# Kernel optimization log

Measured on AMD Instinct MI355X. Metric: run time of the kernel, lower is better.

Reference implementation:

```python
import jax, jax.numpy as jnp
import numpy as np

B, N = 4, 500
C_DIM = 256            # content_dim == feat_channels
G = 4                  # n_groups
P_IN, P_OUT = 32, 128
EFF = C_DIM // G       # 64 = eff_in_dim = eff_out_dim
TOTAL = EFF * EFF + P_IN * P_OUT   # 8192 params per group per query
STRIDES = (8, 16, 32, 64)
LVL_SHAPES = ((100, 160), (50, 80), (25, 40), (13, 20))
TAU = 2.0
LVL_MAP = 3.0          # log2(STRIDES[0]): z -> fpn level index
EPS = 1e-5


def setup_inputs() -> dict:
    key = jax.random.key(0)
    ks = jax.random.split(key, 16)
    feats = [jax.random.normal(ks[i], (B, C_DIM, h, w), jnp.float32)
             for i, (h, w) in enumerate(LVL_SHAPES)]
    query_feat = jax.random.normal(ks[4], (B, N, C_DIM), jnp.float32)
    xy = jax.random.uniform(ks[5], (B, N, 2), jnp.float32, 50.0, 1000.0)
    z = jax.random.uniform(ks[6], (B, N, 1), jnp.float32, 3.0, 6.0)
    r = jax.random.uniform(ks[7], (B, N, 1), jnp.float32, -1.0, 1.0)
    query_xyzr = jnp.concatenate([xy, z, r], -1)
    w_off = jax.random.normal(ks[8], (C_DIM, P_IN * G * 3), jnp.float32) * 0.01
    b_off = jax.random.normal(ks[9], (P_IN * G * 3,), jnp.float32) * 0.1
    w_pg = jax.random.normal(ks[10], (C_DIM, G * TOTAL), jnp.float32) * 0.02
    b_pg = jax.random.normal(ks[11], (G * TOTAL,), jnp.float32) * 0.02
    w_out = jax.random.normal(ks[12], (G * P_OUT * EFF, C_DIM), jnp.float32) * 0.005
    b_out = jnp.zeros((C_DIM,), jnp.float32)
    ln_g = jnp.ones((C_DIM,), jnp.float32)
    ln_b = jnp.zeros((C_DIM,), jnp.float32)
    return dict(feat0=feats[0], feat1=feats[1], feat2=feats[2], feat3=feats[3],
                query_feat=query_feat, query_xyzr=query_xyzr,
                w_off=w_off, b_off=b_off, w_pg=w_pg, b_pg=b_pg,
                w_out=w_out, b_out=b_out, ln_g=ln_g, ln_b=ln_b)


def _ln2d(x):
    # F.layer_norm over last TWO dims, no affine
    mu = x.mean((-2, -1), keepdims=True)
    var = jnp.mean((x - mu) ** 2, (-2, -1), keepdims=True)
    return (x - mu) * jax.lax.rsqrt(var + EPS)


def _bilinear(feat, px, py):
    # torch grid_sample(bilinear, zeros padding, align_corners=False)
    # feat: [BG, H, W, Cg]; px, py: [BG, Q] pixel coords
    BGn, H, W, Cg = feat.shape
    fflat = feat.reshape(BGn, H * W, Cg)
    bidx = jnp.arange(BGn)[:, None]
    x0 = jnp.floor(px)
    y0 = jnp.floor(py)
    wx, wy = px - x0, py - y0
    x0i, y0i = x0.astype(jnp.int32), y0.astype(jnp.int32)

    def corner(xi, yi, w):
        valid = (xi >= 0) & (xi < W) & (yi >= 0) & (yi < H)
        idx = jnp.clip(yi, 0, H - 1) * W + jnp.clip(xi, 0, W - 1)
        return fflat[bidx, idx] * (w * valid)[..., None]

    return (corner(x0i, y0i, (1 - wx) * (1 - wy)) + corner(x0i + 1, y0i, wx * (1 - wy))
            + corner(x0i, y0i + 1, (1 - wx) * wy) + corner(x0i + 1, y0i + 1, wx * wy))


def _forward(feat0, feat1, feat2, feat3, query_feat, query_xyzr,
             w_off, b_off, w_pg, b_pg, w_out, b_out, ln_g, ln_b):
    feats = (feat0, feat1, feat2, feat3)
    # --- make_sample_points ---
    off = (query_feat @ w_off + b_off).reshape(B, N, G * P_IN, 3)
    cc = query_xyzr[..., :2]
    z = query_xyzr[..., 2:3]
    r = query_xyzr[..., 3:4]
    roi_wh = (2.0 ** z) * jnp.concatenate([2.0 ** (-0.5 * r), 2.0 ** (0.5 * r)], -1)  # [B,N,2]
    sample_xy = cc[:, :, None, :] + off[..., :2] * roi_wh[:, :, None, :]   # [B,N,G*P,2]
    sample_lvl = z[:, :, None, 0:1] + off[..., 2:3]                        # [B,N,G*P,1]

    # --- sampling_3d: softmax level weights ---
    lvl = sample_lvl[..., 0] - LVL_MAP                                     # [B,N,G*P]
    grid = jnp.arange(len(STRIDES), dtype=lvl.dtype)
    lw = jax.nn.softmax(-((lvl[..., None] - grid) ** 2) / TAU, axis=-1)    # [B,N,G*P,L]

    # regroup to per-group layout [B*G, N*P, ...]
    sx = sample_xy.reshape(B, N, G, P_IN, 2).transpose(0, 2, 1, 3, 4).reshape(B * G, N * P_IN, 2)
    lw_g = lw.reshape(B, N, G, P_IN, -1).transpose(0, 2, 1, 3, 4).reshape(B * G, N * P_IN, -1)

    sampled = jnp.zeros((B * G, N * P_IN, EFF), jnp.float32)
    for li, (feat, stride) in enumerate(zip(feats, STRIDES)):
        H, W = feat.shape[2], feat.shape[3]
        fg = feat.reshape(B * G, EFF, H, W).transpose(0, 2, 3, 1)  # [BG,H,W,EFF]
        nx = sx[..., 0] / (W * stride) * 2.0 - 1.0
        ny = sx[..., 1] / (H * stride) * 2.0 - 1.0
        px = (nx + 1.0) * 0.5 * W - 0.5
        py = (ny + 1.0) * 0.5 * H - 0.5
        sampled = sampled + _bilinear(fg, px, py) * lw_g[..., li][..., None]
    # [B,N,G,P,EFF]
    x = sampled.reshape(B, G, N, P_IN, EFF).transpose(0, 2, 1, 3, 4)

    # --- AdaptiveMixing ---
    params = (query_feat @ w_pg + b_pg).reshape(B * N, G, TOTAL)
    M = params[..., :EFF * EFF].reshape(B * N, G, EFF, EFF)
    S = params[..., EFF * EFF:].reshape(B * N, G, P_OUT, P_IN)
    out = x.reshape(B * N, G, P_IN, EFF)
    out = jax.nn.relu(_ln2d(jnp.einsum('bgpc,bgcd->bgpd', out, M)))  # channel mix
    out = jax.nn.relu(_ln2d(jnp.einsum('bgop,bgpd->bgod', S, out)))  # spatial mix
    out = out.reshape(B, N, G * P_OUT * EFF) @ w_out + b_out
    q = query_feat + out

    # --- final LayerNorm(content_dim) with affine ---
    mu = q.mean(-1, keepdims=True)
    var = jnp.mean((q - mu) ** 2, -1, keepdims=True)
    return (q - mu) * jax.lax.rsqrt(var + EPS) * ln_g + ln_b


def reference(feat0, feat1, feat2, feat3, query_feat, query_xyzr,
              w_off, b_off, w_pg, b_pg, w_out, b_out, ln_g, ln_b):
    return _forward(feat0, feat1, feat2, feat3, query_feat, query_xyzr,
                    w_off, b_off, w_pg, b_pg, w_out, b_out, ln_g, ln_b)
```

## Files before the change

### kernel.cpp

```cpp
#include <hip/hip_runtime.h>
#include <hip/hip_bf16.h>
#include <cstdint>
#include <cstddef>

#define DI __device__ __forceinline__

#define NN 500
#define NQ 2000
#define GTOT 32768
#define LN_EPS 1e-5f

typedef __attribute__((ext_vector_type(8))) short short8v;
typedef __attribute__((ext_vector_type(4))) float f32x4;
typedef const __attribute__((address_space(1))) void* gp1_t;
typedef __attribute__((address_space(3))) void* lp3_t;

DI unsigned short f2bf(float f){
  unsigned u = __float_as_uint(f);
  return (unsigned short)((u + 0x7fffu + ((u>>16)&1u)) >> 16);
}
DI float bf2f(unsigned short s){ return __uint_as_float(((unsigned)s)<<16); }

DI ushort4 cvt4(float4 a){
  ushort4 r; r.x=f2bf(a.x); r.y=f2bf(a.y); r.z=f2bf(a.z); r.w=f2bf(a.w); return r;
}

DI void bred256(float& s, float& s2, float* red, int tid){
  #pragma unroll
  for(int off=32; off; off>>=1){
    s  += __shfl_xor(s,  off, 64);
    s2 += __shfl_xor(s2, off, 64);
  }
  int w = tid>>6;
  if((tid&63)==0){ red[w*2]=s; red[w*2+1]=s2; }
  __syncthreads();
  s  = red[0]+red[2]+red[4]+red[6];
  s2 = red[1]+red[3]+red[5]+red[7];
  __syncthreads();
}

__global__ __launch_bounds__(384) void k_off(const float* __restrict__ qf,
    const float* __restrict__ xyzr, const float* __restrict__ w_off,
    const float* __restrict__ b_off, float2* __restrict__ xyb, float4* __restrict__ lwb){
  __shared__ float qs[8][256];
  __shared__ float os[8][384];
  int q0 = blockIdx.x*8, tid = threadIdx.x;
  for(int idx=tid; idx<2048; idx+=384){
    int qq = idx>>8, k = idx&255;
    qs[qq][k] = qf[(size_t)(q0+qq)*256 + k];
  }
  __syncthreads();
  {
    int j = tid;
    float acc[8];
    #pragma unroll
    for(int i=0;i<8;i++) acc[i]=0.f;
    for(int k=0;k<256;k++){
      float w = w_off[(size_t)k*384 + j];
      #pragma unroll
      for(int qq=0;qq<8;qq++) acc[qq] += qs[qq][k]*w;
    }
    float bb = b_off[j];
    #pragma unroll
    for(int qq=0;qq<8;qq++) os[qq][j] = acc[qq] + bb;
  }
  __syncthreads();
  for(int idx=tid; idx<1024; idx+=384){
    int qq = idx>>7, gp = idx&127;
    int q = q0+qq;
    float4 xr = *(const float4*)&xyzr[(size_t)q*4];
    float rw = exp2f(xr.z - 0.5f*xr.w);
    float rh = exp2f(xr.z + 0.5f*xr.w);
    float sx = xr.x + os[qq][gp*3+0]*rw;
    float sy = xr.y + os[qq][gp*3+1]*rh;
    float lvl = xr.z + os[qq][gp*3+2] - 3.0f;
    float d0=lvl, d1=lvl-1.f, d2=lvl-2.f, d3=lvl-3.f;
    float e0=-0.5f*d0*d0, e1=-0.5f*d1*d1, e2=-0.5f*d2*d2, e3=-0.5f*d3*d3;
    float m = fmaxf(fmaxf(e0,e1),fmaxf(e2,e3));
    float x0=expf(e0-m), x1=expf(e1-m), x2=expf(e2-m), x3=expf(e3-m);
    float inv = 1.f/(x0+x1+x2+x3);
    xyb[(size_t)q*128+gp] = make_float2(sx,sy);
    lwb[(size_t)q*128+gp] = make_float4(x0*inv, x1*inv, x2*inv, x3*inv);
  }
}

__global__ __launch_bounds__(256) void k_cvtqf(const float* __restrict__ qf,
    unsigned short* __restrict__ qfb){
  int idx = blockIdx.x*256 + threadIdx.x;
  size_t base = (size_t)idx*8;
  int row = idx >> 5;
  ushort4 lo, hi;
  if(row < NQ){
    float4 a = *(const float4*)(qf + base);
    float4 b = *(const float4*)(qf + base + 4);
    lo = cvt4(a); hi = cvt4(b);
  } else {
    lo.x=lo.y=lo.z=lo.w=0; hi.x=hi.y=hi.z=hi.w=0;
  }
  *(ushort4*)(qfb + base) = lo;
  *(ushort4*)(qfb + base + 4) = hi;
}

__global__ __launch_bounds__(256) void k_trcvt(const float* __restrict__ src,
    unsigned short* __restrict__ dst, int R, int C){
  int ctiles = C >> 6;
  int rt = blockIdx.x / ctiles, ct = blockIdx.x % ctiles;
  int r0 = rt<<6, c0 = ct<<6;
  int t = threadIdx.x;
  int tr = t >> 4, tc = t & 15;
  int r = r0 + tr*4, c = c0 + tc*4;
  float4 v0 = *(const float4*)(src + (size_t)(r+0)*C + c);
  float4 v1 = *(const float4*)(src + (size_t)(r+1)*C + c);
  float4 v2 = *(const float4*)(src + (size_t)(r+2)*C + c);
  float4 v3 = *(const float4*)(src + (size_t)(r+3)*C + c);
  ushort4 o0 = make_ushort4(f2bf(v0.x), f2bf(v1.x), f2bf(v2.x), f2bf(v3.x));
  ushort4 o1 = make_ushort4(f2bf(v0.y), f2bf(v1.y), f2bf(v2.y), f2bf(v3.y));
  ushort4 o2 = make_ushort4(f2bf(v0.z), f2bf(v1.z), f2bf(v2.z), f2bf(v3.z));
  ushort4 o3 = make_ushort4(f2bf(v0.w), f2bf(v1.w), f2bf(v2.w), f2bf(v3.w));
  *(ushort4*)(dst + (size_t)(c+0)*R + r) = o0;
  *(ushort4*)(dst + (size_t)(c+1)*R + r) = o1;
  *(ushort4*)(dst + (size_t)(c+2)*R + r) = o2;
  *(ushort4*)(dst + (size_t)(c+3)*R + r) = o3;
}

__global__ __launch_bounds__(256) void k_featT(const float* __restrict__ src,
    unsigned short* __restrict__ dst, int HW, int nb){
  int bg = blockIdx.x / nb, hb = blockIdx.x % nb;
  int b = bg >> 2, g = bg & 3;
  const float* s = src + ((size_t)(b*256 + g*64))*HW;
  unsigned short* d = dst + (size_t)bg*HW*64;
  int t = threadIdx.x;
  int tc = t >> 4, th = t & 15;
  int c = tc*4, hw = hb*64 + th*4;
  if(hw >= HW) return;
  float4 v0 = *(const float4*)(s + (size_t)(c+0)*HW + hw);
  float4 v1 = *(const float4*)(s + (size_t)(c+1)*HW + hw);
  float4 v2 = *(const float4*)(s + (size_t)(c+2)*HW + hw);
  float4 v3 = *(const float4*)(s + (size_t)(c+3)*HW + hw);
  ushort4 o0 = make_ushort4(f2bf(v0.x), f2bf(v1.x), f2bf(v2.x), f2bf(v3.x));
  ushort4 o1 = make_ushort4(f2bf(v0.y), f2bf(v1.y), f2bf(v2.y), f2bf(v3.y));
  ushort4 o2 = make_ushort4(f2bf(v0.z), f2bf(v1.z), f2bf(v2.z), f2bf(v3.z));
  ushort4 o3 = make_ushort4(f2bf(v0.w), f2bf(v1.w), f2bf(v2.w), f2bf(v3.w));
  *(ushort4*)(d + (size_t)(hw+0)*64 + c) = o0;
  *(ushort4*)(d + (size_t)(hw+1)*64 + c) = o1;
  *(ushort4*)(d + (size_t)(hw+2)*64 + c) = o2;
  *(ushort4*)(d + (size_t)(hw+3)*64 + c) = o3;
}

DI f32x4 mfma16(short8v a, short8v b, f32x4 c){
  return __builtin_amdgcn_mfma_f32_16x16x32_bf16(a, b, c, 0, 0, 0);
}

DI int swz32(int c, int r){ return c ^ (r&3) ^ ((r>>2)&3); }

DI void stageG32(const unsigned short* __restrict__ g, size_t row0, size_t ldk,
                 size_t k0, unsigned short* lds, int tid){
  int wv = tid>>6;
  #pragma unroll
  for(int i=0;i<2;i++){
    int e = i*256 + tid;
    int r = e>>2, c = e&3;
    int cs = swz32(c, r);
    const unsigned short* gp = g + (row0 + (size_t)r)*ldk + k0 + (size_t)cs*8;
    unsigned short* lp = lds + (size_t)(i*256 + wv*64)*8;
    __builtin_amdgcn_global_load_lds((gp1_t)(const void*)gp, (lp3_t)(void*)lp, 16, 0, 0);
  }
}

DI short8v frag32(const unsigned short* lds, int row, int q4){
  return *(const short8v*)(lds + (size_t)row*32 + (size_t)swz32(q4, row)*8);
}

DI void mma32(const unsigned short* lsA, const unsigned short* lsB,
              int wm, int wn, int lane, f32x4 acc[4][4]){
  int r15 = lane&15, q4 = lane>>4;
  short8v a[4], b[4];
  #pragma unroll
  for(int i=0;i<4;i++){
    a[i] = frag32(lsA, wm*64 + i*16 + r15, q4);
    b[i] = frag32(lsB, wn*64 + i*16 + r15, q4);
  }
  #pragma unroll
  for(int mi=0;mi<4;mi++)
    #pragma unroll
    for(int ni=0;ni<4;ni++)
      acc[mi][ni] = mfma16(a[mi], b[ni], acc[mi][ni]);
}

DI int xcd_remap(int bid, int nwg){
  return ((bid & 7) * (nwg >> 3)) + (bid >> 3);
}

__global__ __launch_bounds__(256, 4) void k_pgemm_mfma(const unsigned short* __restrict__ qfb,
    const unsigned short* __restrict__ wpgT, const float* __restrict__ b_pg,
    unsigned short* __restrict__ par, int qbase, int qlim, int mtiles){
  __shared__ unsigned short pool[16384];
  int bid = xcd_remap(blockIdx.x, gridDim.x);
  int mt = bid % mtiles, nt = bid / mtiles;
  size_t m0 = (size_t)mt*128, n0 = (size_t)nt*128;
  int tid = threadIdx.x, lane = tid&63, wv = tid>>6;
  int wm = wv>>1, wn = wv&1;
  int r15 = lane&15, q4 = lane>>4;
  f32x4 acc[4][4] = {};
  stageG32(qfb,  qbase+m0, 256, 0, pool, tid);
  stageG32(wpgT, n0,       256, 0, pool + 8192, tid);
  __syncthreads();
  #pragma unroll
  for(int t=0; t<8; t++){
    int co = (t&1)*4096;
    if(t<7){
      int no = ((t&1)^1)*4096;
      stageG32(qfb,  qbase+m0, 256, (size_t)(t+1)*32, pool + no, tid);
      stageG32(wpgT, n0,       256, (size_t)(t+1)*32, pool + 8192 + no, tid);
    }
    mma32(pool + co, pool + 8192 + co, wm, wn, lane, acc);
    __syncthreads();
  }
  unsigned short* es = pool;
  #pragma unroll
  for(int h=0; h<2; ++h){
    if(h) __syncthreads();
    if(wn == h){
      #pragma unroll
      for(int ni=0; ni<4; ni++){
        float bias = b_pg[(int)n0 + wn*64 + ni*16 + r15];
        #pragma unroll
        for(int mi=0; mi<4; mi++)
          #pragma unroll
          for(int j=0; j<4; j++){
            int row = wm*64 + mi*16 + q4*4 + j;
            es[row*72 + ni*16 + r15] = f2bf(acc[mi][ni][j] + bias);
          }
      }
    }
    __syncthreads();
    #pragma unroll
    for(int i=0;i<4;i++){
      int e = i*256 + tid;
      int row = e>>3, c8 = (e&7)*8;
      int rl = (int)m0 + row;
      if(qbase + rl < qlim){
        uint4 v = *(const uint4*)(es + row*72 + c8);
        *(uint4*)&par[(size_t)rl*GTOT + n0 + h*64 + c8] = v;
      }
    }
  }
}

__global__ __launch_bounds__(256, 4) void k_fgemm_mfma(const unsigned short* __restrict__ Ag,
    const unsigned short* __restrict__ woutT, float* __restrict__ part,
    int qbase, int qlim, int mtiles, int kspl){
  __shared__ unsigned short pool[16384];
  int bid = xcd_remap(blockIdx.x, gridDim.x);
  int nt = bid & 1;
  int r2 = bid >> 1;
  int mt = r2 % mtiles, ks = r2 / mtiles;
  size_t m0 = (size_t)mt*128, n0 = (size_t)nt*128;
  int tid = threadIdx.x, lane = tid&63, wv = tid>>6;
  int wm = wv>>1, wn = wv&1;
  f32x4 acc[4][4] = {};
  int klen = GTOT / kspl;
  size_t kbase = (size_t)ks*klen;
  int NT = klen >> 5;
  stageG32(Ag,    m0, GTOT, kbase, pool, tid);
  stageG32(woutT, n0, GTOT, kbase, pool + 8192, tid);
  __syncthreads();
  for(int t=0; t<NT; t++){
    int co = (t&1)*4096;
    if(t+1<NT){
      int no = ((t&1)^1)*4096;
      stageG32(Ag,    m0, GTOT, kbase + (size_t)(t+1)*32, pool + no, tid);
      stageG32(woutT, n0, GTOT, kbase + (size_t)(t+1)*32, pool + 8192 + no, tid);
    }
    mma32(pool + co, pool + 8192 + co, wm, wn, lane, acc);
    __syncthreads();
  }
  float* pp = part + (size_t)ks*NQ*256;
  int r15 = lane&15, q4 = lane>>4;
  #pragma unroll
  for(int mi=0; mi<4; mi++){
    #pragma unroll
    for(int j=0; j<4; j++){
      int rl = (int)m0 + wm*64 + mi*16 + q4*4 + j;
      int q = qbase + rl;
      if(q < qlim){
        #pragma unroll
        for(int ni=0; ni<4; ni++){
          int col = (int)n0 + wn*64 + ni*16 + r15;
          pp[(size_t)q*256 + col] = acc[mi][ni][j];
        }
      }
    }
  }
}

__global__ __launch_bounds__(256) void k_mix(const unsigned short* __restrict__ featT,
    const float2* __restrict__ xyb, const float4* __restrict__ lwb,
    const unsigned short* __restrict__ par, unsigned short* __restrict__ out2,
    int qbase){
  __shared__ __align__(16) char poolA[23040];
  __shared__ __align__(16) unsigned short Ss[128*40];
  __shared__ float red[8];
  float* offW = (float*)poolA;
  unsigned short* xs  = (unsigned short*)(poolA + 4096);
  unsigned short* Ms  = (unsigned short*)(poolA + 4096 + 4608);
  unsigned short* o1t = (unsigned short*)(poolA + 4096 + 4608 + 9216);
  unsigned short* o2s = (unsigned short*)poolA;

  int lq = blockIdx.x >> 2, g = blockIdx.x & 3;
  int q = qbase + lq;
  int b = q / NN;
  int bg = b*4 + g;
  int tid = threadIdx.x;
  int lane = tid & 63, wv = tid >> 6;

  const int HH[4] = {100,50,25,13};
  const int WW[4] = {160,80,40,20};
  const float IS[4] = {0.125f, 0.0625f, 0.03125f, 0.015625f};
  const int LO[4] = {0, 16384000, 20480000, 21504000};

  const unsigned short* pb = par + (size_t)lq*GTOT + (size_t)g*8192;
  uint4 mraw0 = *(const uint4*)(pb + tid*8);
  uint4 mraw1 = *(const uint4*)(pb + 2048 + tid*8);
  uint4 sraw0 = *(const uint4*)(pb + 4096 + tid*8);
  uint4 sraw1 = *(const uint4*)(pb + 6144 + tid*8);

  if(tid < 128){
    int p = tid >> 2, l = tid & 3;
    int pi = q*128 + g*32 + p;
    float2 xy = xyb[pi];
    float lw4 = ((const float*)lwb)[(size_t)pi*4 + l];
    int H = HH[l], W = WW[l];
    float px = xy.x*IS[l] - 0.5f;
    float py = xy.y*IS[l] - 0.5f;
    float xf = floorf(px), yf = floorf(py);
    float wx = px - xf, wy = py - yf;
    int x0 = (int)xf, y0 = (int)yf;
    int x1 = x0 + 1, y1 = y0 + 1;
    bool vx0 = (x0>=0)&&(x0<W), vx1 = (x1>=0)&&(x1<W);
    bool vy0 = (y0>=0)&&(y0<H), vy1 = (y1>=0)&&(y1<H);
    int x0c = min(max(x0,0),W-1), x1c = min(max(x1,0),W-1);
    int y0c = min(max(y0,0),H-1), y1c = min(max(y1,0),H-1);
    int base = LO[l] + bg*H*W*64;
    float* e = offW + tid*8;
    e[0] = __int_as_float(base + (y0c*W + x0c)*64);
    e[1] = __int_as_float(base + (y0c*W + x1c)*64);
    e[2] = __int_as_float(base + (y1c*W + x0c)*64);
    e[3] = __int_as_float(base + (y1c*W + x1c)*64);
    e[4] = (1.f-wx)*(1.f-wy)*lw4*(float)(vx0&&vy0);
    e[5] = wx*(1.f-wy)*lw4*(float)(vx1&&vy0);
    e[6] = (1.f-wx)*wy*lw4*(float)(vx0&&vy1);
    e[7] = wx*wy*lw4*(float)(vx1&&vy1);
  }

  {
    int idx0 = tid*8;
    int c0 = idx0>>6, d0 = idx0&63;
    *(uint4*)(Ms + c0*72 + d0) = mraw0;
    int idx1 = 2048 + tid*8;
    int c1 = idx1>>6, d1 = idx1&63;
    *(uint4*)(Ms + c1*72 + d1) = mraw1;
    int o0 = idx0>>5, p0 = idx0&31;
    *(uint4*)(Ss + o0*40 + p0) = sraw0;
    int o1_ = idx1>>5, p1 = idx1&31;
    *(uint4*)(Ss + o1_*40 + p1) = sraw1;
  }
  __syncthreads();

  {
    int half = lane >> 5, cp = lane & 31;
    const unsigned short* fb_ = featT + cp*2;
    #pragma unroll
    for(int i=0;i<4;i++){
      int p = wv*8 + i*2 + half;
      const float* e = offW + p*32;
      float aLo = 0.f, aHi = 0.f;
      #pragma unroll
      for(int l=0;l<4;l++){
        float4 ea = *(const float4*)(e + l*8);
        float4 eb = *(const float4*)(e + l*8 + 4);
        unsigned u00 = *(const unsigned*)(fb_ + __float_as_int(ea.x));
        unsigned u01 = *(const unsigned*)(fb_ + __float_as_int(ea.y));
        unsigned u10 = *(const unsigned*)(fb_ + __float_as_int(ea.z));
        unsigned u11 = *(const unsigned*)(fb_ + __float_as_int(ea.w));
        aLo += eb.x*__uint_as_float(u00<<16); aHi += eb.x*__uint_as_float(u00&0xffff0000u);
        aLo += eb.y*__uint_as_float(u01<<16); aHi += eb.y*__uint_as_float(u01&0xffff0000u);
        aLo += eb.z*__uint_as_float(u10<<16); aHi += eb.z*__uint_as_float(u10&0xffff0000u);
        aLo += eb.w*__uint_as_float(u11<<16); aHi += eb.w*__uint_as_float(u11&0xffff0000u);
      }
      unsigned lo = f2bf(aLo), hi = f2bf(aHi);
      *(unsigned*)(xs + p*72 + cp*2) = lo | (hi<<16);
    }
  }
  __syncthreads();

  int r = lane & 15, q4 = lane >> 4;

  {
    short8v af00 = *(const short8v*)(xs + r*72 + q4*8);
    short8v af01 = *(const short8v*)(xs + r*72 + 32 + q4*8);
    short8v af10 = *(const short8v*)(xs + (16+r)*72 + q4*8);
    short8v af11 = *(const short8v*)(xs + (16+r)*72 + 32 + q4*8);
    short8v bm0, bm1;
    #pragma unroll
    for(int j=0;j<8;j++){
      bm0[j] = (short)Ms[(8*q4+j)*72 + wv*16 + r];
      bm1[j] = (short)Ms[(32+8*q4+j)*72 + wv*16 + r];
    }
    f32x4 a0 = {}, a1 = {};
    a0 = mfma16(af00, bm0, a0); a0 = mfma16(af01, bm1, a0);
    a1 = mfma16(af10, bm0, a1); a1 = mfma16(af11, bm1, a1);

    float s = 0.f, s2 = 0.f;
    #pragma unroll
    for(int v=0;v<4;v++){ s += a0[v]+a1[v]; s2 += a0[v]*a0[v] + a1[v]*a1[v]; }
    bred256(s, s2, red, tid);
    float mean = s*(1.f/2048.f);
    float var = s2*(1.f/2048.f) - mean*mean;
    float rs = rsqrtf(var + LN_EPS);
    #pragma unroll
    for(int v=0;v<4;v++){
      float f0 = (a0[v]-mean)*rs; f0 = f0>0.f ? f0 : 0.f;
      float f1 = (a1[v]-mean)*rs; f1 = f1>0.f ? f1 : 0.f;
      o1t[(wv*16+r)*40 + 4*q4 + v] = f2bf(f0);
      o1t[(wv*16+r)*40 + 16 + 4*q4 + v] = f2bf(f1);
    }
  }
  __syncthreads();

  {
    short8v sa0 = *(const short8v*)(Ss + ((wv*2+0)*16 + r)*40 + q4*8);
    short8v sa1 = *(const short8v*)(Ss + ((wv*2+1)*16 + r)*40 + q4*8);
    short8v ov0 = *(const short8v*)(o1t + (r)*40 + q4*8);
    short8v ov1 = *(const short8v*)(o1t + (16+r)*40 + q4*8);
    short8v ov2 = *(const short8v*)(o1t + (32+r)*40 + q4*8);
    short8v ov3 = *(const short8v*)(o1t + (48+r)*40 + q4*8);
    f32x4 c2[2][4] = {};
    c2[0][0] = mfma16(sa0, ov0, c2[0][0]); c2[0][1] = mfma16(sa0, ov1, c2[0][1]);
    c2[0][2] = mfma16(sa0, ov2, c2[0][2]); c2[0][3] = mfma16(sa0, ov3, c2[0][3]);
    c2[1][0] = mfma16(sa1, ov0, c2[1][0]); c2[1][1] = mfma16(sa1, ov1, c2[1][1]);
    c2[1][2] = mfma16(sa1, ov2, c2[1][2]); c2[1][3] = mfma16(sa1, ov3, c2[1][3]);

    float s = 0.f, s2 = 0.f;
    #pragma unroll
    for(int m=0;m<2;m++)
      #pragma unroll
      for(int ni=0;ni<4;ni++)
        #pragma unroll
        for(int v=0;v<4;v++){ float x = c2[m][ni][v]; s += x; s2 += x*x; }
    bred256(s, s2, red, tid);
    float mean = s*(1.f/8192.f);
    float var = s2*(1.f/8192.f) - mean*mean;
    float rs = rsqrtf(var + LN_EPS);
    #pragma unroll
    for(int m=0;m<2;m++)
      #pragma unroll
      for(int ni=0;ni<4;ni++)
        #pragma unroll
        for(int v=0;v<4;v++){
          float x = (c2[m][ni][v]-mean)*rs; x = x>0.f ? x : 0.f;
          int o = (wv*2+m)*16 + 4*q4 + v;
          int d = ni*16 + r;
          o2s[o*72 + d] = f2bf(x);
        }
  }
  __syncthreads();

  unsigned short* og = out2 + (size_t)lq*GTOT + (size_t)g*8192;
  #pragma unroll
  for(int i=0;i<32;i++){
    int row = wv*32 + i;
    og[row*64 + lane] = o2s[row*72 + lane];
  }
}

__global__ __launch_bounds__(256) void k_ln(const float* __restrict__ part,
    const float* __restrict__ qf, const float* __restrict__ b_out,
    const float* __restrict__ ln_g, const float* __restrict__ ln_b,
    float* __restrict__ out, int kspl){
  __shared__ float red[8];
  int q = blockIdx.x, j = threadIdx.x;
  float s = qf[(size_t)q*256 + j] + b_out[j];
  for(int ks=0; ks<kspl; ks++) s += part[((size_t)ks*NQ + q)*256 + j];
  float a = s, a2 = s*s;
  bred256(a, a2, red, j);
  float mean = a*(1.f/256.f);
  float var = a2*(1.f/256.f) - mean*mean;
  float rs = rsqrtf(var + LN_EPS);
  out[(size_t)q*256 + j] = (s-mean)*rs*ln_g[j] + ln_b[j];
}

extern "C" void kernel_launch(void* const* d_in, const int* in_sizes, int n_in,
                              void* d_out, int out_size, void* d_ws, size_t ws_size,
                              hipStream_t stream) {
  const float* feat0 = (const float*)d_in[0];
  const float* feat1 = (const float*)d_in[1];
  const float* feat2 = (const float*)d_in[2];
  const float* feat3 = (const float*)d_in[3];
  const float* qf    = (const float*)d_in[4];
  const float* xyzr  = (const float*)d_in[5];
  const float* w_off = (const float*)d_in[6];
  const float* b_off = (const float*)d_in[7];
  const float* w_pg  = (const float*)d_in[8];
  const float* b_pg  = (const float*)d_in[9];
  const float* w_out = (const float*)d_in[10];
  const float* b_out = (const float*)d_in[11];
  const float* ln_g  = (const float*)d_in[12];
  const float* ln_b  = (const float*)d_in[13];

  const int cand_ksp[5] = {32,16,16,16,16};
  const int cand_nc [5] = { 1, 1, 2, 4, 8};
  int KSP=0, NC=0, qcount=0, qpad=0;
  size_t oFEAT=0,oXY=0,oLW=0,oPART=0,oQFB=0,oWPGT=0,oWOUT=0,oPAR=0;
  for(int ci=0; ci<5; ci++){
    size_t o = 0;
    auto al = [&](size_t bytes){ size_t r = o; o = (o + bytes + 255) & ~255ull; return r; };
    size_t tFEAT = al(43540480ull);
    size_t tXY   = al((size_t)NQ*128*8);
    size_t tLW   = al((size_t)NQ*128*16);
    size_t tPART = al((size_t)cand_ksp[ci]*NQ*256*4);
    size_t tQFB  = al((size_t)2048*256*2);
    size_t tWPGT = al((size_t)GTOT*256*2);
    size_t tWOUT = al((size_t)256*GTOT*2);
    int qc = NQ / cand_nc[ci];
    int qp = (qc + 127) & ~127;
    size_t tPAR = al((size_t)qp*GTOT*2);
    if(o <= ws_size){
      KSP=cand_ksp[ci]; NC=cand_nc[ci]; qcount=qc; qpad=qp;
      oFEAT=tFEAT; oXY=tXY; oLW=tLW; oPART=tPART; oQFB=tQFB; oWPGT=tWPGT; oWOUT=tWOUT; oPAR=tPAR;
      break;
    }
  }
  if(NC == 0) return;

  char* ws = (char*)d_ws;
  unsigned short* featT = (unsigned short*)(ws + oFEAT);
  float2* xyb = (float2*)(ws + oXY);
  float4* lwb = (float4*)(ws + oLW);
  float* part = (float*)(ws + oPART);
  unsigned short* qfb  = (unsigned short*)(ws + oQFB);
  unsigned short* wpgT = (unsigned short*)(ws + oWPGT);
  unsigned short* woutT= (unsigned short*)(ws + oWOUT);
  unsigned short* par  = (unsigned short*)(ws + oPAR);
  unsigned short* o2   = par;

  k_off<<<250, 384, 0, stream>>>(qf, xyzr, w_off, b_off, xyb, lwb);
  k_cvtqf<<<256, 256, 0, stream>>>(qf, qfb);
  k_trcvt<<<2048, 256, 0, stream>>>(w_pg,  wpgT, 256, GTOT);
  k_trcvt<<<2048, 256, 0, stream>>>(w_out, woutT, GTOT, 256);
  k_featT<<<16*250, 256, 0, stream>>>(feat0, featT + 0,        16000, 250);
  k_featT<<<16*63,  256, 0, stream>>>(feat1, featT + 16384000, 4000,  63);
  k_featT<<<16*16,  256, 0, stream>>>(feat2, featT + 20480000, 1000,  16);
  k_featT<<<16*5,   256, 0, stream>>>(feat3, featT + 21504000, 260,   5);

  int mtiles = qpad / 128;
  for (int c = 0; c < NC; ++c) {
    int qbase = c * qcount;
    int qlim  = qbase + qcount;
    k_pgemm_mfma<<<mtiles*256, 256, 0, stream>>>(qfb, wpgT, b_pg, par, qbase, qlim, mtiles);
    k_mix<<<qcount*4, 256, 0, stream>>>(featT, xyb, lwb, par, o2, qbase);
    k_fgemm_mfma<<<mtiles*2*KSP, 256, 0, stream>>>(o2, woutT, part, qbase, qlim, mtiles, KSP);
  }
  k_ln<<<NQ, 256, 0, stream>>>(part, qf, b_out, ln_g, ln_b, (float*)d_out, KSP);
}
```

Measured before the change: 329.7 us.

## Transpose via LDS tiles in convert kernels and narrow fgemm N-tile

The weight and feature transpose-convert kernels now stage a 64x64 tile in padded shared memory. This lets both the global reads and the global writes be coalesced, where before each thread did strided 8-byte scattered writes. The final GEMM switches from 128x128 to 128x64 tiles, doubling the grid and shrinking LDS and accumulator use to raise parallelism. The cost is more redundant A-tile loads and an extra block barrier in the transpose kernels.

```diff
diff --git a/kernel.cpp b/kernel.cpp
--- a/kernel.cpp
+++ b/kernel.cpp
@@ -103,48 +103,64 @@
 
 __global__ __launch_bounds__(256) void k_trcvt(const float* __restrict__ src,
     unsigned short* __restrict__ dst, int R, int C){
+  __shared__ unsigned short tile[64*68];
   int ctiles = C >> 6;
   int rt = blockIdx.x / ctiles, ct = blockIdx.x % ctiles;
   int r0 = rt<<6, c0 = ct<<6;
-  int t = threadIdx.x;
-  int tr = t >> 4, tc = t & 15;
-  int r = r0 + tr*4, c = c0 + tc*4;
-  float4 v0 = *(const float4*)(src + (size_t)(r+0)*C + c);
-  float4 v1 = *(const float4*)(src + (size_t)(r+1)*C + c);
-  float4 v2 = *(const float4*)(src + (size_t)(r+2)*C + c);
-  float4 v3 = *(const float4*)(src + (size_t)(r+3)*C + c);
-  ushort4 o0 = make_ushort4(f2bf(v0.x), f2bf(v1.x), f2bf(v2.x), f2bf(v3.x));
-  ushort4 o1 = make_ushort4(f2bf(v0.y), f2bf(v1.y), f2bf(v2.y), f2bf(v3.y));
-  ushort4 o2 = make_ushort4(f2bf(v0.z), f2bf(v1.z), f2bf(v2.z), f2bf(v3.z));
-  ushort4 o3 = make_ushort4(f2bf(v0.w), f2bf(v1.w), f2bf(v2.w), f2bf(v3.w));
-  *(ushort4*)(dst + (size_t)(c+0)*R + r) = o0;
-  *(ushort4*)(dst + (size_t)(c+1)*R + r) = o1;
-  *(ushort4*)(dst + (size_t)(c+2)*R + r) = o2;
-  *(ushort4*)(dst + (size_t)(c+3)*R + r) = o3;
+  int tid = threadIdx.x;
+  #pragma unroll
+  for(int i=0;i<4;i++){
+    int idx = tid + i*256;
+    int r = idx >> 4, c4 = (idx & 15)*4;
+    float4 v = *(const float4*)(src + (size_t)(r0+r)*C + c0 + c4);
+    *(ushort4*)(tile + r*68 + c4) = cvt4(v);
+  }
+  __syncthreads();
+  #pragma unroll
+  for(int i=0;i<4;i++){
+    int idx = tid + i*256;
+    int cc = idx >> 4, r4 = (idx & 15)*4;
+    ushort4 v;
+    v.x = tile[(r4+0)*68 + cc];
+    v.y = tile[(r4+1)*68 + cc];
+    v.z = tile[(r4+2)*68 + cc];
+    v.w = tile[(r4+3)*68 + cc];
+    *(ushort4*)(dst + (size_t)(c0+cc)*R + r0 + r4) = v;
+  }
 }
 
 __global__ __launch_bounds__(256) void k_featT(const float* __restrict__ src,
     unsigned short* __restrict__ dst, int HW, int nb){
+  __shared__ unsigned short tile[64*68];
   int bg = blockIdx.x / nb, hb = blockIdx.x % nb;
   int b = bg >> 2, g = bg & 3;
-  const float* s = src + ((size_t)(b*256 + g*64))*HW;
-  unsigned short* d = dst + (size_t)bg*HW*64;
-  int t = threadIdx.x;
-  int tc = t >> 4, th = t & 15;
-  int c = tc*4, hw = hb*64 + th*4;
-  if(hw >= HW) return;
-  float4 v0 = *(const float4*)(s + (size_t)(c+0)*HW + hw);
-  float4 v1 = *(const float4*)(s + (size_t)(c+1)*HW + hw);
-  float4 v2 = *(const float4*)(s + (size_t)(c+2)*HW + hw);
-  float4 v3 = *(const float4*)(s + (size_t)(c+3)*HW + hw);
-  ushort4 o0 = make_ushort4(f2bf(v0.x), f2bf(v1.x), f2bf(v2.x), f2bf(v3.x));
-  ushort4 o1 = make_ushort4(f2bf(v0.y), f2bf(v1.y), f2bf(v2.y), f2bf(v3.y));
-  ushort4 o2 = make_ushort4(f2bf(v0.z), f2bf(v1.z), f2bf(v2.z), f2bf(v3.z));
-  ushort4 o3 = make_ushort4(f2bf(v0.w), f2bf(v1.w), f2bf(v2.w), f2bf(v3.w));
-  *(ushort4*)(d + (size_t)(hw+0)*64 + c) = o0;
-  *(ushort4*)(d + (size_t)(hw+1)*64 + c) = o1;
-  *(ushort4*)(d + (size_t)(hw+2)*64 + c) = o2;
-  *(ushort4*)(d + (size_t)(hw+3)*64 + c) = o3;
+  const float* s = src + ((size_t)(b*256 + g*64))*HW + hb*64;
+  unsigned short* d = dst + (size_t)bg*HW*64 + (size_t)hb*64*64;
+  int rem = HW - hb*64;
+  int tid = threadIdx.x;
+  #pragma unroll
+  for(int i=0;i<4;i++){
+    int idx = tid + i*256;
+    int c = idx >> 4, h4 = (idx & 15)*4;
+    if(h4 < rem){
+      float4 v = *(const float4*)(s + (size_t)c*HW + h4);
+      *(ushort4*)(tile + c*68 + h4) = cvt4(v);
+    }
+  }
+  __syncthreads();
+  #pragma unroll
+  for(int i=0;i<4;i++){
+    int idx = tid + i*256;
+    int hw = idx >> 4, c4 = (idx & 15)*4;
+    if(hw < rem){
+      ushort4 v;
+      v.x = tile[(c4+0)*68 + hw];
+      v.y = tile[(c4+1)*68 + hw];
+      v.z = tile[(c4+2)*68 + hw];
+      v.w = tile[(c4+3)*68 + hw];
+      *(ushort4*)(d + (size_t)hw*64 + c4) = v;
+    }
+  }
 }
 
 DI f32x4 mfma16(short8v a, short8v b, f32x4 c){
@@ -165,6 +181,16 @@
     unsigned short* lp = lds + (size_t)(i*256 + wv*64)*8;
     __builtin_amdgcn_global_load_lds((gp1_t)(const void*)gp, (lp3_t)(void*)lp, 16, 0, 0);
   }
+}
+
+DI void stageB32(const unsigned short* __restrict__ g, size_t row0, size_t ldk,
+                 size_t k0, unsigned short* lds, int tid){
+  int wv = tid>>6;
+  int r = tid>>2, c = tid&3;
+  int cs = swz32(c, r);
+  const unsigned short* gp = g + (row0 + (size_t)r)*ldk + k0 + (size_t)cs*8;
+  unsigned short* lp = lds + (size_t)(wv*64)*8;
+  __builtin_amdgcn_global_load_lds((gp1_t)(const void*)gp, (lp3_t)(void*)lp, 16, 0, 0);
 }
 
 DI short8v frag32(const unsigned short* lds, int row, int q4){
@@ -250,33 +276,46 @@
 __global__ __launch_bounds__(256, 4) void k_fgemm_mfma(const unsigned short* __restrict__ Ag,
     const unsigned short* __restrict__ woutT, float* __restrict__ part,
     int qbase, int qlim, int mtiles, int kspl){
-  __shared__ unsigned short pool[16384];
+  __shared__ unsigned short pool[12288];
   int bid = xcd_remap(blockIdx.x, gridDim.x);
-  int nt = bid & 1;
-  int r2 = bid >> 1;
+  int nt = bid & 3;
+  int r2 = bid >> 2;
   int mt = r2 % mtiles, ks = r2 / mtiles;
-  size_t m0 = (size_t)mt*128, n0 = (size_t)nt*128;
+  size_t m0 = (size_t)mt*128, n0 = (size_t)nt*64;
   int tid = threadIdx.x, lane = tid&63, wv = tid>>6;
   int wm = wv>>1, wn = wv&1;
-  f32x4 acc[4][4] = {};
+  int r15 = lane&15, q4 = lane>>4;
+  f32x4 acc[4][2] = {};
   int klen = GTOT / kspl;
   size_t kbase = (size_t)ks*klen;
   int NT = klen >> 5;
   stageG32(Ag,    m0, GTOT, kbase, pool, tid);
-  stageG32(woutT, n0, GTOT, kbase, pool + 8192, tid);
+  stageB32(woutT, n0, GTOT, kbase, pool + 8192, tid);
   __syncthreads();
   for(int t=0; t<NT; t++){
-    int co = (t&1)*4096;
+    int coA = (t&1)*4096, coB = (t&1)*2048;
     if(t+1<NT){
-      int no = ((t&1)^1)*4096;
-      stageG32(Ag,    m0, GTOT, kbase + (size_t)(t+1)*32, pool + no, tid);
-      stageG32(woutT, n0, GTOT, kbase + (size_t)(t+1)*32, pool + 8192 + no, tid);
-    }
-    mma32(pool + co, pool + 8192 + co, wm, wn, lane, acc);
+      int noA = ((t&1)^1)*4096, noB = ((t&1)^1)*2048;
+      stageG32(Ag,    m0, GTOT, kbase + (size_t)(t+1)*32, pool + noA, tid);
+      stageB32(woutT, n0, GTOT, kbase + (size_t)(t+1)*32, pool + 8192 + noB, tid);
+    }
+    {
+      const unsigned short* lsA = pool + coA;
+      const unsigned short* lsB = pool + 8192 + coB;
+      short8v a[4], b[2];
+      #pragma unroll
+      for(int i=0;i<4;i++) a[i] = frag32(lsA, wm*64 + i*16 + r15, q4);
+      #pragma unroll
+      for(int i=0;i<2;i++) b[i] = frag32(lsB, wn*32 + i*16 + r15, q4);
+      #pragma unroll
+      for(int mi=0;mi<4;mi++)
+        #pragma unroll
+        for(int ni=0;ni<2;ni++)
+          acc[mi][ni] = mfma16(a[mi], b[ni], acc[mi][ni]);
+    }
     __syncthreads();
   }
   float* pp = part + (size_t)ks*NQ*256;
-  int r15 = lane&15, q4 = lane>>4;
   #pragma unroll
   for(int mi=0; mi<4; mi++){
     #pragma unroll
@@ -285,8 +324,8 @@
       int q = qbase + rl;
       if(q < qlim){
         #pragma unroll
-        for(int ni=0; ni<4; ni++){
-          int col = (int)n0 + wn*64 + ni*16 + r15;
+        for(int ni=0; ni<2; ni++){
+          int col = (int)n0 + wn*32 + ni*16 + r15;
           pp[(size_t)q*256 + col] = acc[mi][ni][j];
         }
       }
@@ -559,7 +598,7 @@
     int qlim  = qbase + qcount;
     k_pgemm_mfma<<<mtiles*256, 256, 0, stream>>>(qfb, wpgT, b_pg, par, qbase, qlim, mtiles);
     k_mix<<<qcount*4, 256, 0, stream>>>(featT, xyb, lwb, par, o2, qbase);
-    k_fgemm_mfma<<<mtiles*2*KSP, 256, 0, stream>>>(o2, woutT, part, qbase, qlim, mtiles, KSP);
+    k_fgemm_mfma<<<mtiles*4*KSP, 256, 0, stream>>>(o2, woutT, part, qbase, qlim, mtiles, KSP);
   }
   k_ln<<<NQ, 256, 0, stream>>>(part, qf, b_out, ln_g, ln_b, (float*)d_out, KSP);
 }
```

Result: faster. 321.7 us (-2.4%).
